# Kernel tuning notes

Measured on AMD Instinct MI355X. Metric: run time of the kernel, lower is better.

## Reference

```python
import jax, jax.numpy as jnp
import numpy as np

IN_F, HID, NCLS = 512, 512, 512
BATCH, W = 32, 2048

def setup_inputs() -> dict:
    key = jax.random.key(0)
    k1, k2, k3, k4, k5 = jax.random.split(key, 5)
    # xavier-ish init for linear weights, stored as (in, out) so we use x @ W + b
    s1 = 1.0 / np.sqrt(IN_F + HID)
    s2 = 1.0 / np.sqrt(HID)
    return {
        "input": jax.random.normal(k1, (BATCH, W, IN_F), dtype=jnp.float32),
        "pre_state": jnp.zeros((W, HID), dtype=jnp.float32),
        "W1": jax.random.uniform(k2, (IN_F + HID, HID), minval=-s1, maxval=s1, dtype=jnp.float32),
        "b1": jax.random.uniform(k3, (HID,), minval=-s1, maxval=s1, dtype=jnp.float32),
        "W2": jax.random.uniform(k4, (HID, NCLS), minval=-s2, maxval=s2, dtype=jnp.float32),
        "b2": jax.random.uniform(k5, (NCLS,), minval=-s2, maxval=s2, dtype=jnp.float32),
    }

def reference(input, pre_state, W1, b1, W2, b2):
    # Sequential recurrence over the leading (batch-as-time) axis.
    def step(state, x_b):            # state: (W, HID), x_b: (W, IN_F)
        tmp = jnp.concatenate([x_b, state], axis=1)       # (W, IN_F+HID)
        hidden = jnp.tanh(tmp @ W1 + b1)                  # (W, HID)
        out_b = jax.nn.softmax(hidden @ W2 + b2, axis=1)  # (W, NCLS)
        # torch code detaches hidden before carrying it forward
        return jax.lax.stop_gradient(hidden), out_b
    final_state, out = jax.lax.scan(step, pre_state, input)
    return out, final_state
```

## Files before the change

kernel.cpp:

```cpp
#include <hip/hip_runtime.h>
#include <hip/hip_bf16.h>
#include <math.h>

#define GLB __attribute__((address_space(1)))
#define LDSAS __attribute__((address_space(3)))

typedef __attribute__((ext_vector_type(8))) short short8;
typedef __attribute__((ext_vector_type(4))) float floatx4;
typedef unsigned short u16;

static __device__ __forceinline__ u16 f2bf(float f) {
  __hip_bfloat16 h = __float2bfloat16(f);
  return __builtin_bit_cast(u16, h);
}
static __device__ __forceinline__ float bf2f(u16 h) {
  return __bfloat162float(__builtin_bit_cast(__hip_bfloat16, h));
}
static __device__ __forceinline__ float tanh_fast(float x) {
  float e = __expf(2.0f * x);
  return 1.0f - 2.0f / (e + 1.0f);
}
static __device__ __forceinline__ floatx4 mfma16(short8 a, short8 b, floatx4 c) {
  return __builtin_amdgcn_mfma_f32_16x16x32_bf16(a, b, c, 0, 0, 0);
}

template <int NCHUNK, int NTHREADS, int L2CPR>
static __device__ __forceinline__ void stage_swz(const u16* __restrict__ g, int ld,
                                                 u16* lds_base, int tid) {
#pragma unroll
  for (int s0 = 0; s0 < NCHUNK; s0 += NTHREADS) {
    int s = s0 + tid;
    int r = s >> L2CPR, c = s & ((1 << L2CPR) - 1);
    const u16* src = g + r * ld + ((c ^ (r & 7)) << 3);
    __builtin_amdgcn_global_load_lds((const GLB unsigned int*)src,
                                     (LDSAS unsigned int*)(lds_base + ((unsigned)(s0 + (tid & ~63)) << 3)),
                                     16, 0, 0);
  }
}

static __device__ __forceinline__ short8 frag_swz(const u16* tile, int row, int kc) {
  return *(const short8*)(tile + row * 64 + ((kc ^ (row & 7)) << 3));
}

__global__ __launch_bounds__(256) void k_prep(const float* __restrict__ W1, const float* __restrict__ W2,
                                              u16* __restrict__ W1x_t, u16* __restrict__ W1h_p,
                                              u16* __restrict__ W2_p) {
  int id = blockIdx.x * 256 + threadIdx.x;
  int m = id >> 15;
  int r = id & 32767;
  if (m == 0) {
    int n = r >> 6, c = r & 63;
    const float* src = W1 + n;
    short8 pk;
#pragma unroll
    for (int j = 0; j < 8; ++j) pk[j] = (short)f2bf(src[(size_t)(c * 8 + j) * 512]);
    *(short8*)(W1x_t + (size_t)n * 512 + c * 8) = pk;
  } else {
    int f = r >> 6, l = r & 63;
    int kc = f >> 5, nf = f & 31;
    int n = (nf << 4) + (l & 15);
    int kb = (kc << 5) + ((l >> 4) << 3);
    const float* src = (m == 1) ? (W1 + (size_t)512 * 512) : W2;
    u16* dst = (m == 1) ? W1h_p : W2_p;
    short8 pk;
#pragma unroll
    for (int e = 0; e < 8; ++e) pk[e] = (short)f2bf(src[(size_t)(kb + e) * 512 + n]);
    *(short8*)(dst + ((size_t)f << 9) + (l << 3)) = pk;
  }
}

__global__ __launch_bounds__(256, 2) void k_phaseA(const float* __restrict__ X,
                                                   const u16* __restrict__ Bt,
                                                   const float* __restrict__ b1,
                                                   u16* __restrict__ Ub) {
  int flat = blockIdx.x;
  int v = ((flat & 7) << 8) + (flat >> 3);
  const int mt = v >> 2, nt = v & 3;
  const int tid = threadIdx.x;
  const int lane = tid & 63, wv = tid >> 6;
  const int wm = wv >> 1, wn = wv & 1;
  const int l15 = lane & 15, lg = lane >> 4;
  __shared__ __align__(16) u16 As[128 * 64];
  __shared__ __align__(16) u16 Bs[128 * 64];
  floatx4 acc[4][4];
  const floatx4 z4 = {0.f, 0.f, 0.f, 0.f};
#pragma unroll
  for (int i = 0; i < 4; ++i)
#pragma unroll
    for (int j = 0; j < 4; ++j) acc[i][j] = z4;

  const float* Ab = X + (size_t)(mt * 128) * 512;
  const u16* Bb = Bt + (size_t)(nt * 128) * 512;

  for (int kt = 0; kt < 8; ++kt) {
#pragma unroll
    for (int s0 = 0; s0 < 1024; s0 += 256) {
      int s = s0 + tid;
      int r = s >> 3, c = s & 7;
      const float* sp = Ab + (size_t)r * 512 + kt * 64 + c * 8;
      float4 f0 = *(const float4*)sp;
      float4 f1 = *(const float4*)(sp + 4);
      short8 pk;
      pk[0] = (short)f2bf(f0.x); pk[1] = (short)f2bf(f0.y);
      pk[2] = (short)f2bf(f0.z); pk[3] = (short)f2bf(f0.w);
      pk[4] = (short)f2bf(f1.x); pk[5] = (short)f2bf(f1.y);
      pk[6] = (short)f2bf(f1.z); pk[7] = (short)f2bf(f1.w);
      *(short8*)(As + r * 64 + ((c ^ (r & 7)) << 3)) = pk;
    }
    stage_swz<1024, 256, 3>(Bb + kt * 64, 512, Bs, tid);
    __syncthreads();
#pragma unroll
    for (int ks = 0; ks < 2; ++ks) {
      int kc = ks * 4 + lg;
      short8 a[4], b[4];
#pragma unroll
      for (int i = 0; i < 4; ++i) a[i] = frag_swz(As, wm * 64 + i * 16 + l15, kc);
#pragma unroll
      for (int i = 0; i < 4; ++i) b[i] = frag_swz(Bs, wn * 64 + i * 16 + l15, kc);
#pragma unroll
      for (int mi = 0; mi < 4; ++mi)
#pragma unroll
        for (int ni = 0; ni < 4; ++ni) acc[mi][ni] = mfma16(a[mi], b[ni], acc[mi][ni]);
    }
    __syncthreads();
  }
  const int r0 = mt * 128 + wm * 64, c0 = nt * 128 + wn * 64;
#pragma unroll
  for (int ni = 0; ni < 4; ++ni) {
    int col = c0 + ni * 16 + l15;
    float bb = b1[col];
#pragma unroll
    for (int mi = 0; mi < 4; ++mi)
#pragma unroll
      for (int j = 0; j < 4; ++j) {
        int row = r0 + mi * 16 + lg * 4 + j;
        Ub[(size_t)row * 512 + col] = f2bf(acc[mi][ni][j] + bb);
      }
  }
}

__global__ __launch_bounds__(512, 2) void k_stepseq(const float* __restrict__ pre,
                                                    const u16* __restrict__ Ub,
                                                    const u16* __restrict__ W1h_p,
                                                    u16* __restrict__ H,
                                                    float* __restrict__ Fs) {
  const int mt = blockIdx.x;
  const int r0 = mt * 16;
  const int tid = threadIdx.x;
  const int lane = tid & 63, wn = tid >> 6;
  const int l15 = lane & 15, lg = lane >> 4;
  __shared__ __align__(16) u16 Ah[16 * 512];
  __shared__ __align__(16) u16 Us[16 * 512];

  const float* Sp = pre + ((size_t)r0 << 9);
#pragma unroll
  for (int s0 = 0; s0 < 1024; s0 += 512) {
    int s = s0 + tid;
    int r = s >> 6, c = s & 63;
    const float* sp = Sp + ((size_t)r << 9) + (c << 3);
    float4 f0 = *(const float4*)sp;
    float4 f1 = *(const float4*)(sp + 4);
    short8 pk;
    pk[0] = (short)f2bf(f0.x); pk[1] = (short)f2bf(f0.y);
    pk[2] = (short)f2bf(f0.z); pk[3] = (short)f2bf(f0.w);
    pk[4] = (short)f2bf(f1.x); pk[5] = (short)f2bf(f1.y);
    pk[6] = (short)f2bf(f1.z); pk[7] = (short)f2bf(f1.w);
    *(short8*)(Ah + (r << 9) + ((c ^ (r & 7)) << 3)) = pk;
  }

  const u16* Wb = W1h_p + ((size_t)(wn * 4) << 9) + (lane << 3);
  short8 breg[9][4];
#pragma unroll
  for (int kc = 0; kc < 9; ++kc)
#pragma unroll
    for (int i = 0; i < 4; ++i)
      breg[kc][i] = *(const short8*)(Wb + ((size_t)(kc * 32 + i) << 9));

  __syncthreads();
  const floatx4 z4 = {0.f, 0.f, 0.f, 0.f};

  for (int t = 0; t < 32; ++t) {
    stage_swz<1024, 512, 6>(Ub + ((size_t)t << 20) + ((size_t)r0 << 9), 512, Us, tid);

    short8 sb[2][4];
#pragma unroll
    for (int d = 0; d < 2; ++d)
#pragma unroll
      for (int i = 0; i < 4; ++i)
        sb[d][i] = *(const short8*)(Wb + ((size_t)((9 + d) * 32 + i) << 9));

    floatx4 acc[4] = {z4, z4, z4, z4};
#pragma unroll
    for (int kc = 0; kc < 16; ++kc) {
      short8 c0, c1, c2, c3;
      if (kc < 9) {
        c0 = breg[kc][0]; c1 = breg[kc][1]; c2 = breg[kc][2]; c3 = breg[kc][3];
      } else {
        const int d = (kc - 9) & 1;
        c0 = sb[d][0]; c1 = sb[d][1]; c2 = sb[d][2]; c3 = sb[d][3];
        if (kc + 2 < 16) {
#pragma unroll
          for (int i = 0; i < 4; ++i)
            sb[d][i] = *(const short8*)(Wb + ((size_t)((kc + 2) * 32 + i) << 9));
        }
      }
      short8 a = *(const short8*)(Ah + (l15 << 9) + ((((kc << 2) + lg) ^ (l15 & 7)) << 3));
      __builtin_amdgcn_s_setprio(1);
      acc[0] = mfma16(a, c0, acc[0]);
      acc[1] = mfma16(a, c1, acc[1]);
      acc[2] = mfma16(a, c2, acc[2]);
      acc[3] = mfma16(a, c3, acc[3]);
      __builtin_amdgcn_s_setprio(0);
    }
    __syncthreads();

    u16* Ht = H + ((size_t)t << 20) + ((size_t)r0 << 9);
#pragma unroll
    for (int ni = 0; ni < 4; ++ni)
#pragma unroll
      for (int j = 0; j < 4; ++j) {
        int row = lg * 4 + j;
        int col = wn * 64 + ni * 16 + l15;
        int ch = col >> 3;
        float uvv = bf2f(Us[(row << 9) + ((ch ^ (row & 7)) << 3) + (col & 7)]);
        float hv = tanh_fast(acc[ni][j] + uvv);
        u16 hb = f2bf(hv);
        Ht[(size_t)row * 512 + col] = hb;
        if (t == 31) Fs[(size_t)(r0 + row) * 512 + col] = hv;
        Ah[(row << 9) + ((ch ^ (row & 7)) << 3) + (col & 7)] = hb;
      }
    __syncthreads();
  }
}

__global__ __launch_bounds__(512, 2) void k_phaseC(const u16* __restrict__ H,
                                                   const u16* __restrict__ W2_p,
                                                   const float* __restrict__ b2,
                                                   float* __restrict__ Out) {
  int bt = ((blockIdx.x & 7) << 7) + (blockIdx.x >> 3);
  const int tid = threadIdx.x, lane = tid & 63, wv = tid >> 6;
  const int wm = wv >> 2, wn = wv & 3;
  const int l15 = lane & 15, lg = lane >> 4;
  __shared__ __align__(16) u16 As[64 * 64];
  __shared__ float redmax[4][64];
  __shared__ float redsum[4][64];
  const floatx4 z4 = {0.f, 0.f, 0.f, 0.f};
  floatx4 acc[2][8];
#pragma unroll
  for (int i = 0; i < 2; ++i)
#pragma unroll
    for (int j = 0; j < 8; ++j) acc[i][j] = z4;

  const u16* Ab = H + (size_t)(bt * 64) * 512;
  const u16* Wb = W2_p + ((size_t)(wn * 8) << 9) + (lane << 3);

  for (int kt = 0; kt < 8; ++kt) {
    stage_swz<512, 512, 3>(Ab + kt * 64, 512, As, tid);
    __syncthreads();
#pragma unroll
    for (int ks = 0; ks < 2; ++ks) {
      int kc = ks * 4 + lg;
      int kcg = kt * 2 + ks;
      short8 a[2], b[8];
#pragma unroll
      for (int i = 0; i < 2; ++i) a[i] = frag_swz(As, wm * 32 + i * 16 + l15, kc);
#pragma unroll
      for (int i = 0; i < 8; ++i) b[i] = *(const short8*)(Wb + ((size_t)(kcg * 32 + i) << 9));
#pragma unroll
      for (int mi = 0; mi < 2; ++mi)
#pragma unroll
        for (int ni = 0; ni < 8; ++ni) acc[mi][ni] = mfma16(a[mi], b[ni], acc[mi][ni]);
    }
    __syncthreads();
  }
  float v[2][8][4];
#pragma unroll
  for (int ni = 0; ni < 8; ++ni) {
    float bb = b2[wn * 128 + ni * 16 + l15];
#pragma unroll
    for (int mi = 0; mi < 2; ++mi)
#pragma unroll
      for (int j = 0; j < 4; ++j) v[mi][ni][j] = acc[mi][ni][j] + bb;
  }
  float mw[2][4];
#pragma unroll
  for (int mi = 0; mi < 2; ++mi)
#pragma unroll
    for (int j = 0; j < 4; ++j) {
      float m = v[mi][0][j];
#pragma unroll
      for (int ni = 1; ni < 8; ++ni) m = fmaxf(m, v[mi][ni][j]);
#pragma unroll
      for (int d = 1; d < 16; d <<= 1) m = fmaxf(m, __shfl_xor(m, d, 64));
      mw[mi][j] = m;
      float s = 0.f;
#pragma unroll
      for (int ni = 0; ni < 8; ++ni) {
        v[mi][ni][j] = __expf(v[mi][ni][j] - m);
        s += v[mi][ni][j];
      }
#pragma unroll
      for (int d = 1; d < 16; d <<= 1) s += __shfl_xor(s, d, 64);
      if (l15 == 0) {
        int row = wm * 32 + mi * 16 + lg * 4 + j;
        redmax[wn][row] = m;
        redsum[wn][row] = s;
      }
    }
  __syncthreads();
#pragma unroll
  for (int mi = 0; mi < 2; ++mi)
#pragma unroll
    for (int j = 0; j < 4; ++j) {
      int row = wm * 32 + mi * 16 + lg * 4 + j;
      float m0 = redmax[0][row], m1 = redmax[1][row], m2 = redmax[2][row], m3 = redmax[3][row];
      float M = fmaxf(fmaxf(m0, m1), fmaxf(m2, m3));
      float S = redsum[0][row] * __expf(m0 - M) + redsum[1][row] * __expf(m1 - M) +
                redsum[2][row] * __expf(m2 - M) + redsum[3][row] * __expf(m3 - M);
      float scale = __expf(mw[mi][j] - M) / S;
#pragma unroll
      for (int ni = 0; ni < 8; ++ni)
        Out[(size_t)(bt * 64 + row) * 512 + wn * 128 + ni * 16 + l15] = v[mi][ni][j] * scale;
    }
}

extern "C" void kernel_launch(void* const* d_in, const int* in_sizes, int n_in,
                              void* d_out, int out_size, void* d_ws, size_t ws_size,
                              hipStream_t stream) {
  const float* input = (const float*)d_in[0];
  const float* pre_state = (const float*)d_in[1];
  const float* W1 = (const float*)d_in[2];
  const float* b1 = (const float*)d_in[3];
  const float* W2 = (const float*)d_in[4];
  const float* b2 = (const float*)d_in[5];

  float* out = (float*)d_out;
  float* final_state = out + (size_t)32 * 2048 * 512;
  u16* Ub = (u16*)d_out;

  u16* ws16 = (u16*)d_ws;
  u16* W1x_t = ws16;
  u16* W1h_p = W1x_t + 262144;
  u16* W2_p  = W1h_p + 262144;
  u16* H     = W2_p + 262144;

  k_prep<<<384, 256, 0, stream>>>(W1, W2, W1x_t, W1h_p, W2_p);
  k_phaseA<<<2048, 256, 0, stream>>>(input, W1x_t, b1, Ub);
  k_stepseq<<<128, 512, 0, stream>>>(pre_state, Ub, W1h_p, H, final_state);
  k_phaseC<<<1024, 512, 0, stream>>>(H, W2_p, b2, out);
}
```

Before: 843.9 us.

## Pre-convert input to bf16 and restructure recurrent step weight pipelining

Adds a standalone kernel that converts the fp32 input to bf16 once, into spare output memory. The input-projection GEMM then stages bf16 tiles with the same swizzled loader it already uses for the weights, instead of re-reading and converting fp32 on every N-tile. In the sequential recurrence kernel, the number of register-resident weight chunks drops from 9 to 8 and the streamed weight prefetch becomes 3-deep. The hidden-state global stores are moved after the barrier so they no longer sit on the critical path. The final state is now written from the bf16-rounded value, and the extra conversion pass adds its own memory traffic.

After: 707.6 us. -16.1%, faster.

```diff
diff --git a/kernel.cpp b/kernel.cpp
--- a/kernel.cpp
+++ b/kernel.cpp
@@ -69,7 +69,19 @@
   }
 }
 
-__global__ __launch_bounds__(256, 2) void k_phaseA(const float* __restrict__ X,
+__global__ __launch_bounds__(256) void k_cvtX(const float* __restrict__ X, u16* __restrict__ Xb) {
+  size_t id = ((size_t)blockIdx.x * 256 + threadIdx.x) * 8;
+  float4 f0 = *(const float4*)(X + id);
+  float4 f1 = *(const float4*)(X + id + 4);
+  short8 pk;
+  pk[0] = (short)f2bf(f0.x); pk[1] = (short)f2bf(f0.y);
+  pk[2] = (short)f2bf(f0.z); pk[3] = (short)f2bf(f0.w);
+  pk[4] = (short)f2bf(f1.x); pk[5] = (short)f2bf(f1.y);
+  pk[6] = (short)f2bf(f1.z); pk[7] = (short)f2bf(f1.w);
+  *(short8*)(Xb + id) = pk;
+}
+
+__global__ __launch_bounds__(256, 2) void k_phaseA(const u16* __restrict__ Xb,
                                                    const u16* __restrict__ Bt,
                                                    const float* __restrict__ b1,
                                                    u16* __restrict__ Ub) {
@@ -89,24 +101,11 @@
 #pragma unroll
     for (int j = 0; j < 4; ++j) acc[i][j] = z4;
 
-  const float* Ab = X + (size_t)(mt * 128) * 512;
+  const u16* Ab = Xb + (size_t)(mt * 128) * 512;
   const u16* Bb = Bt + (size_t)(nt * 128) * 512;
 
   for (int kt = 0; kt < 8; ++kt) {
-#pragma unroll
-    for (int s0 = 0; s0 < 1024; s0 += 256) {
-      int s = s0 + tid;
-      int r = s >> 3, c = s & 7;
-      const float* sp = Ab + (size_t)r * 512 + kt * 64 + c * 8;
-      float4 f0 = *(const float4*)sp;
-      float4 f1 = *(const float4*)(sp + 4);
-      short8 pk;
-      pk[0] = (short)f2bf(f0.x); pk[1] = (short)f2bf(f0.y);
-      pk[2] = (short)f2bf(f0.z); pk[3] = (short)f2bf(f0.w);
-      pk[4] = (short)f2bf(f1.x); pk[5] = (short)f2bf(f1.y);
-      pk[6] = (short)f2bf(f1.z); pk[7] = (short)f2bf(f1.w);
-      *(short8*)(As + r * 64 + ((c ^ (r & 7)) << 3)) = pk;
-    }
+    stage_swz<1024, 256, 3>(Ab + kt * 64, 512, As, tid);
     stage_swz<1024, 256, 3>(Bb + kt * 64, 512, Bs, tid);
     __syncthreads();
 #pragma unroll
@@ -139,11 +138,12 @@
   }
 }
 
-__global__ __launch_bounds__(512, 2) void k_stepseq(const float* __restrict__ pre,
-                                                    const u16* __restrict__ Ub,
-                                                    const u16* __restrict__ W1h_p,
-                                                    u16* __restrict__ H,
-                                                    float* __restrict__ Fs) {
+__global__ __launch_bounds__(512) __attribute__((amdgpu_waves_per_eu(2, 2)))
+void k_stepseq(const float* __restrict__ pre,
+               const u16* __restrict__ Ub,
+               const u16* __restrict__ W1h_p,
+               u16* __restrict__ H,
+               float* __restrict__ Fs) {
   const int mt = blockIdx.x;
   const int r0 = mt * 16;
   const int tid = threadIdx.x;
@@ -169,9 +169,9 @@
   }
 
   const u16* Wb = W1h_p + ((size_t)(wn * 4) << 9) + (lane << 3);
-  short8 breg[9][4];
-#pragma unroll
-  for (int kc = 0; kc < 9; ++kc)
+  short8 breg[8][4];
+#pragma unroll
+  for (int kc = 0; kc < 8; ++kc)
 #pragma unroll
     for (int i = 0; i < 4; ++i)
       breg[kc][i] = *(const short8*)(Wb + ((size_t)(kc * 32 + i) << 9));
@@ -182,27 +182,32 @@
   for (int t = 0; t < 32; ++t) {
     stage_swz<1024, 512, 6>(Ub + ((size_t)t << 20) + ((size_t)r0 << 9), 512, Us, tid);
 
-    short8 sb[2][4];
-#pragma unroll
-    for (int d = 0; d < 2; ++d)
+    short8 sb[3][4];
+#pragma unroll
+    for (int d = 0; d < 3; ++d)
 #pragma unroll
       for (int i = 0; i < 4; ++i)
-        sb[d][i] = *(const short8*)(Wb + ((size_t)((9 + d) * 32 + i) << 9));
+        sb[d][i] = *(const short8*)(Wb + ((size_t)((8 + d) * 32 + i) << 9));
 
     floatx4 acc[4] = {z4, z4, z4, z4};
 #pragma unroll
-    for (int kc = 0; kc < 16; ++kc) {
-      short8 c0, c1, c2, c3;
-      if (kc < 9) {
-        c0 = breg[kc][0]; c1 = breg[kc][1]; c2 = breg[kc][2]; c3 = breg[kc][3];
-      } else {
-        const int d = (kc - 9) & 1;
-        c0 = sb[d][0]; c1 = sb[d][1]; c2 = sb[d][2]; c3 = sb[d][3];
-        if (kc + 2 < 16) {
-#pragma unroll
-          for (int i = 0; i < 4; ++i)
-            sb[d][i] = *(const short8*)(Wb + ((size_t)((kc + 2) * 32 + i) << 9));
-        }
+    for (int kc = 0; kc < 8; ++kc) {
+      short8 a = *(const short8*)(Ah + (l15 << 9) + ((((kc << 2) + lg) ^ (l15 & 7)) << 3));
+      __builtin_amdgcn_s_setprio(1);
+      acc[0] = mfma16(a, breg[kc][0], acc[0]);
+      acc[1] = mfma16(a, breg[kc][1], acc[1]);
+      acc[2] = mfma16(a, breg[kc][2], acc[2]);
+      acc[3] = mfma16(a, breg[kc][3], acc[3]);
+      __builtin_amdgcn_s_setprio(0);
+    }
+#pragma unroll
+    for (int kc = 8; kc < 16; ++kc) {
+      const int d = (kc - 8) % 3;
+      short8 c0 = sb[d][0], c1 = sb[d][1], c2 = sb[d][2], c3 = sb[d][3];
+      if (kc + 3 < 16) {
+#pragma unroll
+        for (int i = 0; i < 4; ++i)
+          sb[d][i] = *(const short8*)(Wb + ((size_t)((kc + 3) * 32 + i) << 9));
       }
       short8 a = *(const short8*)(Ah + (l15 << 9) + ((((kc << 2) + lg) ^ (l15 & 7)) << 3));
       __builtin_amdgcn_s_setprio(1);
@@ -214,7 +219,7 @@
     }
     __syncthreads();
 
-    u16* Ht = H + ((size_t)t << 20) + ((size_t)r0 << 9);
+    u16 hb[16];
 #pragma unroll
     for (int ni = 0; ni < 4; ++ni)
 #pragma unroll
@@ -224,12 +229,23 @@
         int ch = col >> 3;
         float uvv = bf2f(Us[(row << 9) + ((ch ^ (row & 7)) << 3) + (col & 7)]);
         float hv = tanh_fast(acc[ni][j] + uvv);
-        u16 hb = f2bf(hv);
-        Ht[(size_t)row * 512 + col] = hb;
-        if (t == 31) Fs[(size_t)(r0 + row) * 512 + col] = hv;
-        Ah[(row << 9) + ((ch ^ (row & 7)) << 3) + (col & 7)] = hb;
-      }
-    __syncthreads();
+        u16 h16 = f2bf(hv);
+        hb[ni * 4 + j] = h16;
+        Ah[(row << 9) + ((ch ^ (row & 7)) << 3) + (col & 7)] = h16;
+      }
+    __syncthreads();
+
+    u16* Ht = H + ((size_t)t << 20) + ((size_t)r0 << 9);
+#pragma unroll
+    for (int ni = 0; ni < 4; ++ni)
+#pragma unroll
+      for (int j = 0; j < 4; ++j) {
+        int row = lg * 4 + j;
+        int col = wn * 64 + ni * 16 + l15;
+        u16 h16 = hb[ni * 4 + j];
+        Ht[(size_t)row * 512 + col] = h16;
+        if (t == 31) Fs[(size_t)(r0 + row) * 512 + col] = bf2f(h16);
+      }
   }
 }
 
@@ -337,6 +353,7 @@
   float* out = (float*)d_out;
   float* final_state = out + (size_t)32 * 2048 * 512;
   u16* Ub = (u16*)d_out;
+  u16* Xb = (u16*)d_out + (size_t)32 * 2048 * 512;
 
   u16* ws16 = (u16*)d_ws;
   u16* W1x_t = ws16;
@@ -345,7 +362,8 @@
   u16* H     = W2_p + 262144;
 
   k_prep<<<384, 256, 0, stream>>>(W1, W2, W1x_t, W1h_p, W2_p);
-  k_phaseA<<<2048, 256, 0, stream>>>(input, W1x_t, b1, Ub);
+  k_cvtX<<<16384, 256, 0, stream>>>(input, Xb);
+  k_phaseA<<<2048, 256, 0, stream>>>(Xb, W1x_t, b1, Ub);
   k_stepseq<<<128, 512, 0, stream>>>(pre_state, Ub, W1h_p, H, final_state);
   k_phaseC<<<1024, 512, 0, stream>>>(H, W2_p, b2, out);
 }
```
